# Optimization experiments

Measured on AMD Instinct MI355X. Metric: run time of the kernel, lower is better.

Reference implementation:

```python
import jax, jax.numpy as jnp
import numpy as np

B, C, H, W = 2, 512, 32, 32
HEADS = 8      # attention heads
GROUPS = 8     # offset groups (defaults to heads)
DH = 64        # dim_head
DF = 4         # downsample_factor
OFF_SCALE = 4.0
EPS = 1e-5


def _bn(t, gamma, beta):
    # eval-mode BatchNorm2d with running_mean=0, running_var=1
    s = gamma / jnp.sqrt(1.0 + EPS)
    return t * s[None, :, None, None] + beta[None, :, None, None]


def _gconv1x1(t, w):
    # grouped 1x1 conv (bias-free); w: (GROUPS, out_per_group, in_per_group)
    b, c, h, ww = t.shape
    o = jnp.einsum('bgci,goc->bgoi', t.reshape(b, GROUPS, c // GROUPS, h * ww), w)
    return o.reshape(b, GROUPS * w.shape[1], h, ww)


def _grid_sample(img, grid):
    # F.grid_sample: bilinear, padding_mode='zeros', align_corners=False
    # img: (N,Ci,Hi,Wi); grid: (N,Hg,Wg,2), grid[...,0]=x, grid[...,1]=y in [-1,1]
    N, Ci, Hi, Wi = img.shape
    gx = (grid[..., 0] + 1.0) * (Wi / 2.0) - 0.5
    gy = (grid[..., 1] + 1.0) * (Hi / 2.0) - 0.5
    x0 = jnp.floor(gx)
    y0 = jnp.floor(gy)
    wx = gx - x0
    wy = gy - y0

    def gather(im, ix, iy):
        valid = (ix >= 0) & (ix < Wi) & (iy >= 0) & (iy < Hi)
        ixc = jnp.clip(ix, 0, Wi - 1).astype(jnp.int32)
        iyc = jnp.clip(iy, 0, Hi - 1).astype(jnp.int32)
        return im[:, iyc, ixc] * valid[None].astype(im.dtype)

    def sample_one(im, x0, y0, wx, wy):
        v00 = gather(im, x0, y0)
        v01 = gather(im, x0 + 1, y0)
        v10 = gather(im, x0, y0 + 1)
        v11 = gather(im, x0 + 1, y0 + 1)
        wx = wx[None]
        wy = wy[None]
        return (v00 * (1 - wx) * (1 - wy) + v01 * wx * (1 - wy)
                + v10 * (1 - wx) * wy + v11 * wx * wy)

    return jax.vmap(sample_one)(img, x0, y0, wx, wy)


def _forward(x, bn1_g, bn1_b, bn2_g, bn2_b, qw, kw, vw, out_w, out_b,
             off_dw_w, off_dw_b, off_pw_w,
             cpb_w1, cpb_b1, cpb_w2, cpb_b2, cpb_w3, cpb_b3,
             mlp_w1, mlp_b1, mlp_w2, mlp_b2):
    b = x.shape[0]
    xn = _bn(x, bn1_g, bn1_b)
    # ---- deformable attention ----
    q = _gconv1x1(xn, qw)                                   # (b, 512, H, W)
    qg = q.reshape(b * GROUPS, DH, H, W)
    # to_offsets: depthwise conv k=6, s=4, p=1 -> GELU -> 1x1(64->2) -> tanh * offset_scale
    off = jax.lax.conv_general_dilated(
        qg, off_dw_w, (DF, DF), ((1, 1), (1, 1)),
        dimension_numbers=('NCHW', 'OIHW', 'NCHW'), feature_group_count=DH)
    off = jax.nn.gelu(off + off_dw_b[None, :, None, None], approximate=False)
    off = jnp.tanh(jnp.einsum('bchw,oc->bohw', off, off_pw_w)) * OFF_SCALE   # (b*G, 2, Hd, Wd)
    Hd, Wd = off.shape[-2], off.shape[-1]
    gy, gx = jnp.meshgrid(jnp.arange(Hd, dtype=x.dtype), jnp.arange(Wd, dtype=x.dtype), indexing='ij')
    vx = gx[None] + off[:, 0]
    vy = gy[None] + off[:, 1]
    # normalize_grid (lucidrains): first comp by (Hd-1), second by (Wd-1)
    nx = 2.0 * vx / max(Hd - 1, 1) - 1.0
    ny = 2.0 * vy / max(Wd - 1, 1) - 1.0
    vgrid_scaled = jnp.stack((nx, ny), axis=-1)             # (b*G, Hd, Wd, 2)
    kv = _grid_sample(xn.reshape(b * GROUPS, DH, H, W), vgrid_scaled)
    kv = kv.reshape(b, GROUPS * DH, Hd, Wd)
    k = _gconv1x1(kv, kw)
    v = _gconv1x1(kv, vw)
    scale = DH ** -0.5
    qh = q.reshape(b, HEADS, DH, H * W).transpose(0, 1, 3, 2) * scale    # (b,h,i,d)
    kh = k.reshape(b, HEADS, DH, Hd * Wd).transpose(0, 1, 3, 2)          # (b,h,j,d)
    vh = v.reshape(b, HEADS, DH, Hd * Wd).transpose(0, 1, 3, 2)
    # continuous relative position bias (CPB)
    qgy, qgx = jnp.meshgrid(jnp.arange(H, dtype=x.dtype), jnp.arange(W, dtype=x.dtype), indexing='ij')
    grid_q = jnp.stack((2.0 * qgx / max(H - 1, 1) - 1.0,
                        2.0 * qgy / max(W - 1, 1) - 1.0), axis=-1).reshape(1, H * W, 2)
    grid_kv = vgrid_scaled.reshape(b * GROUPS, Hd * Wd, 2)
    pos = grid_q[:, :, None, :] - grid_kv[:, None, :, :]    # (b*G, i, j, 2)
    bias = jnp.sign(pos) * jnp.log1p(jnp.abs(pos))
    bias = jax.nn.relu(bias @ cpb_w1 + cpb_b1)
    bias = jax.nn.relu(bias @ cpb_w2 + cpb_b2)
    bias = (bias @ cpb_w3 + cpb_b3).reshape(b, GROUPS, H * W, Hd * Wd)   # heads//groups == 1
    sim = jnp.einsum('bhid,bhjd->bhij', qh, kh) + bias
    attn = jax.nn.softmax(sim, axis=-1)
    out = jnp.einsum('bhij,bhjd->bhid', attn, vh)
    out = out.transpose(0, 1, 3, 2).reshape(b, HEADS * DH, H, W)
    out = jnp.einsum('bchw,oc->bohw', out, out_w) + out_b[None, :, None, None]
    x = x + out
    # ---- conv1x1 MLP ----
    xn2 = _bn(x, bn2_g, bn2_b)
    h1 = jax.nn.gelu(jnp.einsum('bchw,oc->bohw', xn2, mlp_w1) + mlp_b1[None, :, None, None],
                     approximate=False)
    return x + jnp.einsum('bchw,oc->bohw', h1, mlp_w2) + mlp_b2[None, :, None, None]


def setup_inputs():
    ks = jax.random.split(jax.random.key(0), 16)
    w = lambda k, shape: jax.random.normal(k, shape, dtype=jnp.float32) * 0.02
    return {
        'x': jax.random.normal(ks[0], (B, C, H, W), dtype=jnp.float32),
        'bn1_g': jnp.ones((C,), jnp.float32),
        'bn1_b': jnp.zeros((C,), jnp.float32),
        'bn2_g': jnp.ones((C,), jnp.float32),
        'bn2_b': jnp.zeros((C,), jnp.float32),
        'qw': w(ks[1], (GROUPS, DH, C // GROUPS)),
        'kw': w(ks[2], (GROUPS, DH, C // GROUPS)),
        'vw': w(ks[3], (GROUPS, DH, C // GROUPS)),
        'out_w': w(ks[4], (C, HEADS * DH)),
        'out_b': jnp.zeros((C,), jnp.float32),
        'off_dw_w': w(ks[5], (DH, 1, 6, 6)),
        'off_dw_b': jnp.zeros((DH,), jnp.float32),
        'off_pw_w': w(ks[6], (2, DH)),
        'cpb_w1': w(ks[7], (2, 128)),
        'cpb_b1': jnp.zeros((128,), jnp.float32),
        'cpb_w2': w(ks[8], (128, 128)),
        'cpb_b2': jnp.zeros((128,), jnp.float32),
        'cpb_w3': w(ks[9], (128, 1)),
        'cpb_b3': jnp.zeros((1,), jnp.float32),
        'mlp_w1': w(ks[10], (4 * C, C)),
        'mlp_b1': jnp.zeros((4 * C,), jnp.float32),
        'mlp_w2': w(ks[11], (C, 4 * C)),
        'mlp_b2': jnp.zeros((C,), jnp.float32),
    }


def reference(x, bn1_g, bn1_b, bn2_g, bn2_b, qw, kw, vw, out_w, out_b,
              off_dw_w, off_dw_b, off_pw_w,
              cpb_w1, cpb_b1, cpb_w2, cpb_b2, cpb_w3, cpb_b3,
              mlp_w1, mlp_b1, mlp_w2, mlp_b2):
    return _forward(x, bn1_g, bn1_b, bn2_g, bn2_b, qw, kw, vw, out_w, out_b,
                    off_dw_w, off_dw_b, off_pw_w,
                    cpb_w1, cpb_b1, cpb_w2, cpb_b2, cpb_w3, cpb_b3,
                    mlp_w1, mlp_b1, mlp_w2, mlp_b2)
```

## Files before the change

kernel.cpp:

```cpp
#include <hip/hip_runtime.h>
#include <hip/hip_bf16.h>
#include <math.h>

#define BB 2
#define CC 512
#define HH 32
#define WW 32
#define HWP 1024
#define GG 8
#define DH 64
#define HD 8
#define WD 8
#define JJ 64
#define BG 16
#define EPS 1e-5f

typedef __attribute__((ext_vector_type(8))) short short8;
typedef __attribute__((ext_vector_type(4))) short s16x4;
typedef __attribute__((ext_vector_type(4))) float f32x4;
typedef __attribute__((ext_vector_type(4))) unsigned short u16x4;
typedef __attribute__((ext_vector_type(4))) unsigned int u32x4;

static __device__ __forceinline__ short f2bf(float x) {
    unsigned u = __builtin_bit_cast(unsigned, x);
    u += 0x7FFFu + ((u >> 16) & 1u);
    return (short)(u >> 16);
}
static __device__ __forceinline__ float bf2f(unsigned short h) {
    return __builtin_bit_cast(float, (unsigned)h << 16);
}

__global__ void k_wpack(const float* __restrict__ qw, const float* __restrict__ ow,
                        const float* __restrict__ w1, const float* __restrict__ w2,
                        const float* __restrict__ cw2, unsigned short* __restrict__ wp,
                        unsigned short* __restrict__ w2p) {
    int idx = blockIdx.x * 256 + threadIdx.x;
    if (idx < 2392064) {
        float v;
        if (idx < 32768) v = qw[idx];
        else if (idx < 294912) v = ow[idx - 32768];
        else if (idx < 1343488) v = w1[idx - 294912];
        else v = w2[idx - 1343488];
        wp[idx] = (unsigned short)f2bf(v);
    } else if (idx < 2408448) {
        int i2 = idx - 2392064;
        int k = i2 >> 7, n = i2 & 127;
        int dest = ((((n >> 4) * 4 + (k >> 5)) * 64) + (((k >> 3) & 3) * 16) + (n & 15)) * 8 + (k & 7);
        w2p[dest] = (unsigned short)f2bf(cw2[i2]);
    }
}

__global__ __launch_bounds__(256) void k_qgemm(
    const float* __restrict__ x, const float* __restrict__ g1,
    const float* __restrict__ b1, const unsigned short* __restrict__ qwp,
    unsigned short* __restrict__ qt) {
    __shared__ __align__(16) short As[64][72];
    __shared__ __align__(16) short Bs[64][72];
    int blk = blockIdx.x;
    int bg = blk >> 4, nt = blk & 15;
    int b = bg >> 3, g = bg & 7;
    int i0 = nt * 64;
    int tid = threadIdx.x, lane = tid & 63, wv = tid >> 6;
    int wm = (wv >> 1) * 32, wn = (wv & 1) * 32;
    int l15 = lane & 15, quad = lane >> 4;
    const float invs = 1.0f / sqrtf(1.0f + EPS);
    {
        int c4 = (tid & 15) * 4;
        int ob = tid >> 4;
#pragma unroll
        for (int p = 0; p < 4; p++) {
            int o = ob + p * 16;
            u16x4 v = *(const u16x4*)(qwp + (size_t)(g * 64 + o) * 64 + c4);
            *(u16x4*)&As[o][c4] = v;
        }
    }
    {
        int i4 = (tid & 15) * 4;
        int cb = tid >> 4;
#pragma unroll
        for (int p = 0; p < 4; p++) {
            int c = cb + p * 16;
            f32x4 v = *(const f32x4*)(x + (size_t)(b * CC + g * 64 + c) * HWP + i0 + i4);
            float sc = g1[g * 64 + c] * invs;
            float sh = b1[g * 64 + c];
            Bs[i4 + 0][c] = f2bf(fmaf(v.x, sc, sh));
            Bs[i4 + 1][c] = f2bf(fmaf(v.y, sc, sh));
            Bs[i4 + 2][c] = f2bf(fmaf(v.z, sc, sh));
            Bs[i4 + 3][c] = f2bf(fmaf(v.w, sc, sh));
        }
    }
    __syncthreads();
    f32x4 acc[2][2];
#pragma unroll
    for (int a = 0; a < 2; a++)
#pragma unroll
        for (int c = 0; c < 2; c++) acc[a][c] = (f32x4){0.f, 0.f, 0.f, 0.f};
#pragma unroll
    for (int ks = 0; ks < 2; ks++) {
        short8 af0 = *(const short8*)&As[wm + l15][ks * 32 + quad * 8];
        short8 af1 = *(const short8*)&As[wm + 16 + l15][ks * 32 + quad * 8];
        short8 bf0 = *(const short8*)&Bs[wn + l15][ks * 32 + quad * 8];
        short8 bf1 = *(const short8*)&Bs[wn + 16 + l15][ks * 32 + quad * 8];
        acc[0][0] = __builtin_amdgcn_mfma_f32_16x16x32_bf16(af0, bf0, acc[0][0], 0, 0, 0);
        acc[0][1] = __builtin_amdgcn_mfma_f32_16x16x32_bf16(af0, bf1, acc[0][1], 0, 0, 0);
        acc[1][0] = __builtin_amdgcn_mfma_f32_16x16x32_bf16(af1, bf0, acc[1][0], 0, 0, 0);
        acc[1][1] = __builtin_amdgcn_mfma_f32_16x16x32_bf16(af1, bf1, acc[1][1], 0, 0, 0);
    }
    __syncthreads();
#pragma unroll
    for (int im = 0; im < 2; im++)
#pragma unroll
        for (int r = 0; r < 4; r++) {
            int m = wm + im * 16 + quad * 4 + r;
#pragma unroll
            for (int in_ = 0; in_ < 2; in_++) {
                int n = wn + in_ * 16 + l15;
                As[n][m] = f2bf(acc[im][in_][r]);
            }
        }
    __syncthreads();
    {
        int n = tid >> 2;
        int c0 = (tid & 3) * 16;
        short8 a = *(const short8*)&As[n][c0];
        short8 c = *(const short8*)&As[n][c0 + 8];
        unsigned short* dst = qt + ((size_t)bg * 1024 + i0 + n) * 64 + c0;
        *(short8*)dst = a;
        *(short8*)(dst + 8) = c;
    }
}

__global__ __launch_bounds__(64) void k_offskv(
    const unsigned short* __restrict__ qt, const float* __restrict__ dww,
    const float* __restrict__ dwb, const float* __restrict__ pw,
    const float* __restrict__ x, const float* __restrict__ g1,
    const float* __restrict__ b1, const float* __restrict__ kw,
    const float* __restrict__ vw, float* __restrict__ vgrid,
    float* __restrict__ kk, float* __restrict__ vv) {
    __shared__ float sm[64];
    int blk = blockIdx.x;
    int bg = blk >> 6;
    int hd = (blk >> 3) & 7;
    int wd = blk & 7;
    int g = bg & 7, b = bg >> 3;
    int ch = threadIdx.x;
    const unsigned short* qb = qt + (size_t)bg * 65536;
    float acc = 0.f;
#pragma unroll
    for (int kh = 0; kh < 6; kh++) {
        int hin = hd * 4 - 1 + kh;
        if (hin < 0 || hin >= HH) continue;
#pragma unroll
        for (int kw_ = 0; kw_ < 6; kw_++) {
            int win = wd * 4 - 1 + kw_;
            if (win < 0 || win >= WW) continue;
            acc = fmaf(bf2f(qb[(hin * WW + win) * 64 + ch]), dww[ch * 36 + kh * 6 + kw_], acc);
        }
    }
    acc += dwb[ch];
    float ge = 0.5f * acc * (1.0f + erff(acc * 0.7071067811865475f));
    float p0 = ge * pw[ch];
    float p1 = ge * pw[64 + ch];
#pragma unroll
    for (int off = 32; off; off >>= 1) {
        p0 += __shfl_xor(p0, off);
        p1 += __shfl_xor(p1, off);
    }
    float nx = 2.0f * ((float)wd + tanhf(p0) * 4.0f) / 7.0f - 1.0f;
    float ny = 2.0f * ((float)hd + tanhf(p1) * 4.0f) / 7.0f - 1.0f;
    if (ch == 0) {
        vgrid[blk * 2] = nx;
        vgrid[blk * 2 + 1] = ny;
    }
    {
        int cg = g * 64 + ch;
        const float invs = 1.0f / sqrtf(1.0f + EPS);
        float s = g1[cg] * invs;
        float bv = b1[cg];
        float gx = (nx + 1.0f) * 16.0f - 0.5f;
        float gy = (ny + 1.0f) * 16.0f - 0.5f;
        float x0f = floorf(gx), y0f = floorf(gy);
        float wx = gx - x0f, wy = gy - y0f;
        int x0 = (int)x0f, y0 = (int)y0f;
        const float* im = x + (size_t)(b * CC + cg) * HWP;
        float sx = 0.f, sw = 0.f;
        float w00 = (1 - wx) * (1 - wy), w01 = wx * (1 - wy);
        float w10 = (1 - wx) * wy, w11 = wx * wy;
        if (x0 >= 0 && x0 < WW && y0 >= 0 && y0 < HH)                 { sx += w00 * im[y0 * WW + x0];           sw += w00; }
        if (x0 + 1 >= 0 && x0 + 1 < WW && y0 >= 0 && y0 < HH)         { sx += w01 * im[y0 * WW + x0 + 1];       sw += w01; }
        if (x0 >= 0 && x0 < WW && y0 + 1 >= 0 && y0 + 1 < HH)         { sx += w10 * im[(y0 + 1) * WW + x0];     sw += w10; }
        if (x0 + 1 >= 0 && x0 + 1 < WW && y0 + 1 >= 0 && y0 + 1 < HH) { sx += w11 * im[(y0 + 1) * WW + x0 + 1]; sw += w11; }
        sm[ch] = s * sx + bv * sw;
    }
    __syncthreads();
    int j = blk & 63;
    const float* kwr = kw + (size_t)(g * 64 + ch) * 64;
    const float* vwr = vw + (size_t)(g * 64 + ch) * 64;
    float ak = 0.f, av = 0.f;
#pragma unroll
    for (int c = 0; c < 64; c++) {
        float tv = sm[c];
        ak = fmaf(tv, kwr[c], ak);
        av = fmaf(tv, vwr[c], av);
    }
    kk[(size_t)bg * 4096 + j * 64 + ch] = ak;
    vv[(size_t)bg * 4096 + j * 64 + ch] = av;
}

__global__ __launch_bounds__(256) void k_cpb(
    const float* __restrict__ vgrid, const unsigned short* __restrict__ w2p,
    const float* __restrict__ w1, const float* __restrict__ b1,
    const float* __restrict__ b2, const float* __restrict__ w3,
    const float* __restrict__ b3, unsigned short* __restrict__ bias) {
    __shared__ __align__(16) short w2fs[16384];
    int tid = threadIdx.x;
    {
        const u32x4* src = (const u32x4*)w2p;
        u32x4* dst = (u32x4*)w2fs;
        for (int c = tid; c < 2048; c += 256) dst[c] = src[c];
    }
    float bias3 = b3[0];
    __syncthreads();

    int lane = tid & 63;
    int wv = tid >> 6;
    int l15 = lane & 15;
    int quad = lane >> 4;

#pragma unroll 1
    for (int it = 0; it < 4; it++) {
        int p = (blockIdx.x * 4 + it) * 4 + wv;
        int pu = __builtin_amdgcn_readfirstlane(p);
        int cofs = (int)((unsigned)pu >> 20);
        int bg = p >> 11;
        int i = (p >> 1) & 1023;
        int jbase = (p & 1) * 32;
        int hi = i >> 5, wi = i & 31;
        float qx = 2.0f * (float)wi / 31.0f - 1.0f;
        float qy = 2.0f * (float)hi / 31.0f - 1.0f;

        int jA = jbase + l15;
        float gkxA = vgrid[(bg * 64 + jA) * 2];
        float gkyA = vgrid[(bg * 64 + jA) * 2 + 1];
        float gkxB = vgrid[(bg * 64 + jA + 16) * 2];
        float gkyB = vgrid[(bg * 64 + jA + 16) * 2 + 1];
        float p0 = qx - gkxA, p1 = qy - gkyA;
        float s0a = copysignf(log1pf(fabsf(p0)), p0);
        float s1a = copysignf(log1pf(fabsf(p1)), p1);
        p0 = qx - gkxB; p1 = qy - gkyB;
        float s0b = copysignf(log1pf(fabsf(p0)), p0);
        float s1b = copysignf(log1pf(fabsf(p1)), p1);

        short8 hA[4], hB[4];
#pragma unroll
        for (int kc = 0; kc < 4; kc++) {
            f32x4 cu0 = *(const f32x4*)(w1 + cofs + kc * 32 + quad * 8);
            f32x4 cu1 = *(const f32x4*)(w1 + cofs + kc * 32 + quad * 8 + 4);
            f32x4 cv0 = *(const f32x4*)(w1 + cofs + 128 + kc * 32 + quad * 8);
            f32x4 cv1 = *(const f32x4*)(w1 + cofs + 128 + kc * 32 + quad * 8 + 4);
            f32x4 cb0 = *(const f32x4*)(b1 + cofs + kc * 32 + quad * 8);
            f32x4 cb1 = *(const f32x4*)(b1 + cofs + kc * 32 + quad * 8 + 4);
            u32x4 pa, pb;
#pragma unroll
            for (int j2 = 0; j2 < 4; j2++) {
                int e0 = 2 * j2, e1 = 2 * j2 + 1;
                float u0 = (e0 < 4) ? cu0[e0] : cu1[e0 - 4];
                float u1 = (e1 < 4) ? cu0[e1] : cu1[e1 - 4];
                float v0 = (e0 < 4) ? cv0[e0] : cv1[e0 - 4];
                float v1 = (e1 < 4) ? cv0[e1] : cv1[e1 - 4];
                float c0 = (e0 < 4) ? cb0[e0] : cb1[e0 - 4];
                float c1 = (e1 < 4) ? cb0[e1] : cb1[e1 - 4];
                unsigned a0 = __builtin_bit_cast(unsigned,
                    fmaxf(fmaf(s0a, u0, fmaf(s1a, v0, c0)), 0.f)) + 0x8000u;
                unsigned a1 = __builtin_bit_cast(unsigned,
                    fmaxf(fmaf(s0a, u1, fmaf(s1a, v1, c1)), 0.f)) + 0x8000u;
                pa[j2] = __builtin_amdgcn_perm(a1, a0, 0x07060302);
                unsigned b0 = __builtin_bit_cast(unsigned,
                    fmaxf(fmaf(s0b, u0, fmaf(s1b, v0, c0)), 0.f)) + 0x8000u;
                unsigned b1_ = __builtin_bit_cast(unsigned,
                    fmaxf(fmaf(s0b, u1, fmaf(s1b, v1, c1)), 0.f)) + 0x8000u;
                pb[j2] = __builtin_amdgcn_perm(b1_, b0, 0x07060302);
            }
            hA[kc] = __builtin_bit_cast(short8, pa);
            hB[kc] = __builtin_bit_cast(short8, pb);
        }

        float psumA = 0.f, psumB = 0.f;
#pragma unroll 2
        for (int nt = 0; nt < 8; nt++) {
            f32x4 accA = (f32x4){0.f, 0.f, 0.f, 0.f};
            f32x4 accB = (f32x4){0.f, 0.f, 0.f, 0.f};
#pragma unroll
            for (int kc = 0; kc < 4; kc++) {
                short8 af = *(const short8*)(w2fs + (((nt * 4 + kc) * 64) + lane) * 8);
                accA = __builtin_amdgcn_mfma_f32_16x16x32_bf16(af, hA[kc], accA, 0, 0, 0);
                accB = __builtin_amdgcn_mfma_f32_16x16x32_bf16(af, hB[kc], accB, 0, 0, 0);
            }
            f32x4 b2q = *(const f32x4*)(b2 + cofs + nt * 16 + quad * 4);
            f32x4 w3q = *(const f32x4*)(w3 + cofs + nt * 16 + quad * 4);
#pragma unroll
            for (int r = 0; r < 4; r++) {
                psumA = fmaf(fmaxf(accA[r] + b2q[r], 0.f), w3q[r], psumA);
                psumB = fmaf(fmaxf(accB[r] + b2q[r], 0.f), w3q[r], psumB);
            }
        }
        psumA += __shfl_xor(psumA, 16);
        psumA += __shfl_xor(psumA, 32);
        psumB += __shfl_xor(psumB, 16);
        psumB += __shfl_xor(psumB, 32);
        if (quad == 0) {
            bias[(size_t)(p * 2 + 0) * 16 + l15] = (unsigned short)f2bf(psumA + bias3);
            bias[(size_t)(p * 2 + 1) * 16 + l15] = (unsigned short)f2bf(psumB + bias3);
        }
    }
}

__global__ __launch_bounds__(256) void k_attn(
    const unsigned short* __restrict__ qt, const float* __restrict__ kk,
    const float* __restrict__ vv, const unsigned short* __restrict__ bias,
    unsigned short* __restrict__ ao) {
    __shared__ __align__(16) short Ks[64][72];
    __shared__ __align__(16) short Vt[64][72];
    __shared__ __align__(16) short Qs[64][72];
    __shared__ __align__(16) short Ps[4][16][72];
    int blk = blockIdx.x;
    int bg = blk >> 4;
    int chunk = blk & 15;
    int i0 = chunk * 64;
    int b = bg >> 3, g = bg & 7;
    int tid = threadIdx.x, lane = tid & 63, wv = tid >> 6;
    int l15 = lane & 15, quad = lane >> 4;

    const float* kbase = kk + (size_t)bg * 4096;
    const float* vbase = vv + (size_t)bg * 4096;
#pragma unroll
    for (int it = 0; it < 4; it++) {
        int e4 = it * 1024 + tid * 4;
        int j = e4 >> 6, d = e4 & 63;
        f32x4 k4 = *(const f32x4*)(kbase + e4);
        s16x4 s = {f2bf(k4.x), f2bf(k4.y), f2bf(k4.z), f2bf(k4.w)};
        *(s16x4*)&Ks[j][d] = s;
        f32x4 v4 = *(const f32x4*)(vbase + e4);
        Vt[d + 0][j] = f2bf(v4.x);
        Vt[d + 1][j] = f2bf(v4.y);
        Vt[d + 2][j] = f2bf(v4.z);
        Vt[d + 3][j] = f2bf(v4.w);
    }
    {
        const unsigned short* qtb = qt + ((size_t)bg * 1024 + i0) * 64;
#pragma unroll
        for (int it = 0; it < 4; it++) {
            int e4 = it * 1024 + tid * 4;
            int i = e4 >> 6, d = e4 & 63;
            u16x4 v = *(const u16x4*)(qtb + e4);
            *(u16x4*)&Qs[i][d] = v;
        }
    }
    __syncthreads();

    int iw = wv * 16;
    f32x4 Sacc[4];
#pragma unroll
    for (int nt = 0; nt < 4; nt++) Sacc[nt] = (f32x4){0.f, 0.f, 0.f, 0.f};
#pragma unroll
    for (int ks = 0; ks < 2; ks++) {
        short8 aq = *(const short8*)&Qs[iw + l15][quad * 8 + ks * 32];
#pragma unroll
        for (int nt = 0; nt < 4; nt++) {
            short8 bk = *(const short8*)&Ks[nt * 16 + l15][quad * 8 + ks * 32];
            Sacc[nt] = __builtin_amdgcn_mfma_f32_16x16x32_bf16(aq, bk, Sacc[nt], 0, 0, 0);
        }
    }
    const unsigned short* bp = bias + ((size_t)bg * 1024 + i0 + iw + quad * 4) * 64 + l15;
    float Sv[4][4];
#pragma unroll
    for (int nt = 0; nt < 4; nt++)
#pragma unroll
        for (int r = 0; r < 4; r++)
            Sv[nt][r] = fmaf(Sacc[nt][r], 0.125f, bf2f(bp[r * 64 + nt * 16]));
#pragma unroll
    for (int r = 0; r < 4; r++) {
        float m = fmaxf(fmaxf(Sv[0][r], Sv[1][r]), fmaxf(Sv[2][r], Sv[3][r]));
        m = fmaxf(m, __shfl_xor(m, 1));
        m = fmaxf(m, __shfl_xor(m, 2));
        m = fmaxf(m, __shfl_xor(m, 4));
        m = fmaxf(m, __shfl_xor(m, 8));
        float l = 0.f;
#pragma unroll
        for (int nt = 0; nt < 4; nt++) { Sv[nt][r] = expf(Sv[nt][r] - m); l += Sv[nt][r]; }
        l += __shfl_xor(l, 1);
        l += __shfl_xor(l, 2);
        l += __shfl_xor(l, 4);
        l += __shfl_xor(l, 8);
        float inv = 1.0f / l;
#pragma unroll
        for (int nt = 0; nt < 4; nt++)
            Ps[wv][quad * 4 + r][nt * 16 + l15] = f2bf(Sv[nt][r] * inv);
    }
    f32x4 Oacc[4];
#pragma unroll
    for (int nt = 0; nt < 4; nt++) Oacc[nt] = (f32x4){0.f, 0.f, 0.f, 0.f};
#pragma unroll
    for (int ks = 0; ks < 2; ks++) {
        short8 ap = *(const short8*)&Ps[wv][l15][quad * 8 + ks * 32];
#pragma unroll
        for (int nt = 0; nt < 4; nt++) {
            short8 bv = *(const short8*)&Vt[nt * 16 + l15][quad * 8 + ks * 32];
            Oacc[nt] = __builtin_amdgcn_mfma_f32_16x16x32_bf16(ap, bv, Oacc[nt], 0, 0, 0);
        }
    }
    __syncthreads();
#pragma unroll
    for (int nt = 0; nt < 4; nt++) {
        s16x4 o4 = {f2bf(Oacc[nt][0]), f2bf(Oacc[nt][1]), f2bf(Oacc[nt][2]), f2bf(Oacc[nt][3])};
        *(s16x4*)&Qs[nt * 16 + l15][iw + quad * 4] = o4;
    }
    __syncthreads();
    {
        int d = tid >> 2;
        int ic = (tid & 3) * 16;
        short8 a = *(const short8*)&Qs[d][ic];
        short8 c = *(const short8*)&Qs[d][ic + 8];
        unsigned short* dst = ao + (size_t)(b * CC + g * 64 + d) * HWP + i0 + ic;
        *(short8*)dst = a;
        *(short8*)(dst + 8) = c;
    }
}

template<int EPI, int KD, int BK, int MT>
__global__ __launch_bounds__(256) void k_gemm(
    const unsigned short* __restrict__ A, const unsigned short* __restrict__ Bh,
    const float* __restrict__ resid, const float* __restrict__ bias,
    void* __restrict__ outp, unsigned short* __restrict__ out2,
    const float* __restrict__ bns, const float* __restrict__ bnb) {
    constexpr int MM = MT * 64;
    constexpr int KV4 = BK / 4;
    constexpr int RP = 256 / KV4;
    constexpr int NA = 64 / RP;
    constexpr int NB = BK / 16;
    __shared__ __align__(16) short As[64][BK + 8];
    __shared__ __align__(16) short Bs[64][BK + 8];
    int tid = threadIdx.x;
    int blk = blockIdx.x;
    int mt = blk & (MT - 1);
    int nb = blk / MT;
    int bb = nb >> 4, nt = nb & 15;
    int m0 = mt * 64, i0 = nt * 64;
    int lane = tid & 63, wv = tid >> 6;
    int wm = (wv >> 1) * 32, wn = (wv & 1) * 32;
    int l15 = lane & 15, quad = lane >> 4;
    const unsigned short* Af = A + (size_t)m0 * KD;
    const float invs = 1.0f / sqrtf(1.0f + EPS);
    int kk4 = (tid & (KV4 - 1)) * 4;
    int myb = tid / KV4;
    int i4 = (tid & 15) * 4;
    int kyb8 = (tid >> 4) * NB;

    f32x4 acc[2][2];
#pragma unroll
    for (int a = 0; a < 2; a++)
#pragma unroll
        for (int c = 0; c < 2; c++) acc[a][c] = (f32x4){0.f, 0.f, 0.f, 0.f};

    u16x4 ra[NA], rb[NB];
#pragma unroll
    for (int p = 0; p < NA; p++)
        ra[p] = *(const u16x4*)(Af + (size_t)(myb + p * RP) * KD + kk4);
#pragma unroll
    for (int p = 0; p < NB; p++)
        rb[p] = *(const u16x4*)(Bh + (size_t)bb * KD * HWP + (size_t)(kyb8 + p) * HWP + i0 + i4);

    for (int k0 = 0; k0 < KD; k0 += BK) {
        __syncthreads();
#pragma unroll
        for (int p = 0; p < NA; p++)
            *(u16x4*)&As[myb + p * RP][kk4] = ra[p];
#pragma unroll
        for (int q = 0; q < 4; q++) {
            u32x4 w;
#pragma unroll
            for (int j = 0; j < 4; j++) {
                unsigned lo = ((const unsigned*)&rb[2 * j])[q >> 1];
                unsigned hi = ((const unsigned*)&rb[2 * j + 1])[q >> 1];
                w[j] = (q & 1) ? __builtin_amdgcn_perm(hi, lo, 0x07060302)
                               : __builtin_amdgcn_perm(hi, lo, 0x05040100);
            }
            *(u32x4*)&Bs[i4 + q][kyb8] = w;
        }
        __syncthreads();
        int kn = k0 + BK;
        if (kn < KD) {
#pragma unroll
            for (int p = 0; p < NA; p++)
                ra[p] = *(const u16x4*)(Af + (size_t)(myb + p * RP) * KD + kn + kk4);
#pragma unroll
            for (int p = 0; p < NB; p++)
                rb[p] = *(const u16x4*)(Bh + (size_t)bb * KD * HWP + (size_t)(kn + kyb8 + p) * HWP + i0 + i4);
        }
#pragma unroll
        for (int ks = 0; ks < BK / 32; ks++) {
            short8 af0 = *(const short8*)&As[wm + l15][ks * 32 + quad * 8];
            short8 af1 = *(const short8*)&As[wm + 16 + l15][ks * 32 + quad * 8];
            short8 bf0 = *(const short8*)&Bs[wn + l15][ks * 32 + quad * 8];
            short8 bf1 = *(const short8*)&Bs[wn + 16 + l15][ks * 32 + quad * 8];
            acc[0][0] = __builtin_amdgcn_mfma_f32_16x16x32_bf16(af0, bf0, acc[0][0], 0, 0, 0);
            acc[0][1] = __builtin_amdgcn_mfma_f32_16x16x32_bf16(af0, bf1, acc[0][1], 0, 0, 0);
            acc[1][0] = __builtin_amdgcn_mfma_f32_16x16x32_bf16(af1, bf0, acc[1][0], 0, 0, 0);
            acc[1][1] = __builtin_amdgcn_mfma_f32_16x16x32_bf16(af1, bf1, acc[1][1], 0, 0, 0);
        }
    }

    float* outF = (float*)outp;
    unsigned short* outH = (unsigned short*)outp;
#pragma unroll
    for (int im = 0; im < 2; im++) {
#pragma unroll
        for (int r = 0; r < 4; r++) {
            int m = m0 + wm + im * 16 + quad * 4 + r;
            float bv = bias[m];
#pragma unroll
            for (int in_ = 0; in_ < 2; in_++) {
                int n = i0 + wn + in_ * 16 + l15;
                size_t idx = ((size_t)bb * MM + m) * HWP + n;
                float v = acc[im][in_][r] + bv;
                if constexpr (EPI == 1) {
                    float ge = 0.5f * v * (1.0f + erff(v * 0.7071067811865475f));
                    outH[idx] = (unsigned short)f2bf(ge);
                } else if constexpr (EPI == 3) {
                    float vr = v + resid[idx];
                    outF[idx] = vr;
                    out2[idx] = (unsigned short)f2bf(fmaf(vr, bns[m] * invs, bnb[m]));
                } else {
                    outF[idx] = v + resid[idx];
                }
            }
        }
    }
}

extern "C" void kernel_launch(void* const* d_in, const int* in_sizes, int n_in,
                              void* d_out, int out_size, void* d_ws, size_t ws_size,
                              hipStream_t stream) {
    const float* x      = (const float*)d_in[0];
    const float* bn1_g  = (const float*)d_in[1];
    const float* bn1_b  = (const float*)d_in[2];
    const float* bn2_g  = (const float*)d_in[3];
    const float* bn2_b  = (const float*)d_in[4];
    const float* qw     = (const float*)d_in[5];
    const float* kw     = (const float*)d_in[6];
    const float* vw     = (const float*)d_in[7];
    const float* out_w  = (const float*)d_in[8];
    const float* out_b  = (const float*)d_in[9];
    const float* off_dw_w = (const float*)d_in[10];
    const float* off_dw_b = (const float*)d_in[11];
    const float* off_pw_w = (const float*)d_in[12];
    const float* cpb_w1 = (const float*)d_in[13];
    const float* cpb_b1 = (const float*)d_in[14];
    const float* cpb_w2 = (const float*)d_in[15];
    const float* cpb_b2 = (const float*)d_in[16];
    const float* cpb_w3 = (const float*)d_in[17];
    const float* cpb_b3 = (const float*)d_in[18];
    const float* mlp_w1 = (const float*)d_in[19];
    const float* mlp_b1 = (const float*)d_in[20];
    const float* mlp_w2 = (const float*)d_in[21];
    const float* mlp_b2 = (const float*)d_in[22];

    float* ws = (float*)d_ws;
    unsigned short* qt = (unsigned short*)(ws + 1048576);
    float* vgrid = ws + 2097152;
    float* kk    = ws + 2164736;
    float* vv    = ws + 2230272;
    unsigned short* w2p = (unsigned short*)(ws + 2295808);
    unsigned short* ao  = (unsigned short*)(ws + 2312192);
    unsigned short* xn2 = (unsigned short*)(ws + 2836480);
    float* xo    = ws + 3360768;
    float* h1of  = ws + 4409344;
    unsigned short* biasb = (unsigned short*)h1of;
    unsigned short* h1o = (unsigned short*)h1of;
    unsigned short* wp  = (unsigned short*)(ws + 6506496);
    unsigned short* qwp  = wp;
    unsigned short* owp  = wp + 32768;
    unsigned short* w1p  = wp + 294912;
    unsigned short* w2mp = wp + 1343488;

    hipLaunchKernelGGL(k_wpack, dim3(9408), dim3(256), 0, stream,
                       qw, out_w, mlp_w1, mlp_w2, cpb_w2, wp, w2p);
    hipLaunchKernelGGL(k_qgemm, dim3(256), dim3(256), 0, stream, x, bn1_g, bn1_b, qwp, qt);
    hipLaunchKernelGGL(k_offskv, dim3(1024), dim3(64), 0, stream,
                       qt, off_dw_w, off_dw_b, off_pw_w, x, bn1_g, bn1_b, kw, vw,
                       vgrid, kk, vv);
    hipLaunchKernelGGL(k_cpb, dim3(2048), dim3(256), 0, stream,
                       vgrid, w2p, cpb_w1, cpb_b1, cpb_b2, cpb_w3, cpb_b3, biasb);
    hipLaunchKernelGGL(k_attn, dim3(256), dim3(256), 0, stream, qt, kk, vv, biasb, ao);
    k_gemm<3, 512, 128, 8><<<dim3(256), dim3(256), 0, stream>>>(
        owp, ao, x, out_b, xo, xn2, bn2_g, bn2_b);
    k_gemm<1, 512, 128, 32><<<dim3(1024), dim3(256), 0, stream>>>(
        w1p, xn2, nullptr, mlp_b1, h1o, nullptr, nullptr, nullptr);
    k_gemm<2, 2048, 128, 8><<<dim3(256), dim3(256), 0, stream>>>(
        w2mp, h1o, xo, mlp_b2, d_out, nullptr, nullptr, nullptr);
}
```

Before: 239.5 us.

## Transpose k/v/depthwise weights for coalesced reads and store K/V as bf16

Result: faster. 234.2 us (-2.2%).

```diff
diff --git a/kernel.cpp b/kernel.cpp
--- a/kernel.cpp
+++ b/kernel.cpp
@@ -32,8 +32,11 @@
 
 __global__ void k_wpack(const float* __restrict__ qw, const float* __restrict__ ow,
                         const float* __restrict__ w1, const float* __restrict__ w2,
-                        const float* __restrict__ cw2, unsigned short* __restrict__ wp,
-                        unsigned short* __restrict__ w2p) {
+                        const float* __restrict__ cw2, const float* __restrict__ kw,
+                        const float* __restrict__ vw, const float* __restrict__ dww,
+                        unsigned short* __restrict__ wp, unsigned short* __restrict__ w2p,
+                        float* __restrict__ kwt, float* __restrict__ vwt,
+                        float* __restrict__ dwt) {
     int idx = blockIdx.x * 256 + threadIdx.x;
     if (idx < 2392064) {
         float v;
@@ -47,6 +50,18 @@
         int k = i2 >> 7, n = i2 & 127;
         int dest = ((((n >> 4) * 4 + (k >> 5)) * 64) + (((k >> 3) & 3) * 16) + (n & 15)) * 8 + (k & 7);
         w2p[dest] = (unsigned short)f2bf(cw2[i2]);
+    } else if (idx < 2441216) {
+        int i2 = idx - 2408448;
+        int o = i2 & 63, c = (i2 >> 6) & 63, g = i2 >> 12;
+        kwt[i2] = kw[(size_t)(g * 64 + o) * 64 + c];
+    } else if (idx < 2473984) {
+        int i2 = idx - 2441216;
+        int o = i2 & 63, c = (i2 >> 6) & 63, g = i2 >> 12;
+        vwt[i2] = vw[(size_t)(g * 64 + o) * 64 + c];
+    } else if (idx < 2476288) {
+        int i2 = idx - 2473984;
+        int ch = i2 & 63, k = i2 >> 6;
+        dwt[i2] = dww[ch * 36 + k];
     }
 }
 
@@ -131,12 +146,12 @@
 }
 
 __global__ __launch_bounds__(64) void k_offskv(
-    const unsigned short* __restrict__ qt, const float* __restrict__ dww,
+    const unsigned short* __restrict__ qt, const float* __restrict__ dwt,
     const float* __restrict__ dwb, const float* __restrict__ pw,
     const float* __restrict__ x, const float* __restrict__ g1,
-    const float* __restrict__ b1, const float* __restrict__ kw,
-    const float* __restrict__ vw, float* __restrict__ vgrid,
-    float* __restrict__ kk, float* __restrict__ vv) {
+    const float* __restrict__ b1, const float* __restrict__ kwt,
+    const float* __restrict__ vwt, float* __restrict__ vgrid,
+    unsigned short* __restrict__ kkh, unsigned short* __restrict__ vvh) {
     __shared__ float sm[64];
     int blk = blockIdx.x;
     int bg = blk >> 6;
@@ -154,7 +169,8 @@
         for (int kw_ = 0; kw_ < 6; kw_++) {
             int win = wd * 4 - 1 + kw_;
             if (win < 0 || win >= WW) continue;
-            acc = fmaf(bf2f(qb[(hin * WW + win) * 64 + ch]), dww[ch * 36 + kh * 6 + kw_], acc);
+            acc = fmaf(bf2f(qb[(hin * WW + win) * 64 + ch]),
+                       dwt[(kh * 6 + kw_) * 64 + ch], acc);
         }
     }
     acc += dwb[ch];
@@ -194,17 +210,17 @@
     }
     __syncthreads();
     int j = blk & 63;
-    const float* kwr = kw + (size_t)(g * 64 + ch) * 64;
-    const float* vwr = vw + (size_t)(g * 64 + ch) * 64;
+    const float* kwr = kwt + g * 4096 + ch;
+    const float* vwr = vwt + g * 4096 + ch;
     float ak = 0.f, av = 0.f;
 #pragma unroll
     for (int c = 0; c < 64; c++) {
         float tv = sm[c];
-        ak = fmaf(tv, kwr[c], ak);
-        av = fmaf(tv, vwr[c], av);
-    }
-    kk[(size_t)bg * 4096 + j * 64 + ch] = ak;
-    vv[(size_t)bg * 4096 + j * 64 + ch] = av;
+        ak = fmaf(tv, kwr[c * 64], ak);
+        av = fmaf(tv, vwr[c * 64], av);
+    }
+    kkh[(size_t)bg * 4096 + j * 64 + ch] = (unsigned short)f2bf(ak);
+    vvh[(size_t)bg * 4096 + j * 64 + ch] = (unsigned short)f2bf(av);
 }
 
 __global__ __launch_bounds__(256) void k_cpb(
@@ -316,8 +332,8 @@
 }
 
 __global__ __launch_bounds__(256) void k_attn(
-    const unsigned short* __restrict__ qt, const float* __restrict__ kk,
-    const float* __restrict__ vv, const unsigned short* __restrict__ bias,
+    const unsigned short* __restrict__ qt, const unsigned short* __restrict__ kkh,
+    const unsigned short* __restrict__ vvh, const unsigned short* __restrict__ bias,
     unsigned short* __restrict__ ao) {
     __shared__ __align__(16) short Ks[64][72];
     __shared__ __align__(16) short Vt[64][72];
@@ -331,20 +347,34 @@
     int tid = threadIdx.x, lane = tid & 63, wv = tid >> 6;
     int l15 = lane & 15, quad = lane >> 4;
 
-    const float* kbase = kk + (size_t)bg * 4096;
-    const float* vbase = vv + (size_t)bg * 4096;
-#pragma unroll
-    for (int it = 0; it < 4; it++) {
-        int e4 = it * 1024 + tid * 4;
-        int j = e4 >> 6, d = e4 & 63;
-        f32x4 k4 = *(const f32x4*)(kbase + e4);
-        s16x4 s = {f2bf(k4.x), f2bf(k4.y), f2bf(k4.z), f2bf(k4.w)};
-        *(s16x4*)&Ks[j][d] = s;
-        f32x4 v4 = *(const f32x4*)(vbase + e4);
-        Vt[d + 0][j] = f2bf(v4.x);
-        Vt[d + 1][j] = f2bf(v4.y);
-        Vt[d + 2][j] = f2bf(v4.z);
-        Vt[d + 3][j] = f2bf(v4.w);
+    const unsigned short* kbase = kkh + (size_t)bg * 4096;
+    const unsigned short* vbase = vvh + (size_t)bg * 4096;
+#pragma unroll
+    for (int it = 0; it < 2; it++) {
+        int e8 = (it * 256 + tid) * 8;
+        int j = e8 >> 6, d = e8 & 63;
+        u32x4 v = *(const u32x4*)(kbase + e8);
+        *(u32x4*)&Ks[j][d] = v;
+    }
+    if (tid < 128) {
+        int d0 = (tid & 15) * 4;
+        int jb = (tid >> 4) * 8;
+        u16x4 rb[8];
+#pragma unroll
+        for (int p = 0; p < 8; p++)
+            rb[p] = *(const u16x4*)(vbase + (jb + p) * 64 + d0);
+#pragma unroll
+        for (int q = 0; q < 4; q++) {
+            u32x4 w;
+#pragma unroll
+            for (int jj = 0; jj < 4; jj++) {
+                unsigned lo = ((const unsigned*)&rb[2 * jj])[q >> 1];
+                unsigned hi = ((const unsigned*)&rb[2 * jj + 1])[q >> 1];
+                w[jj] = (q & 1) ? __builtin_amdgcn_perm(hi, lo, 0x07060302)
+                                : __builtin_amdgcn_perm(hi, lo, 0x05040100);
+            }
+            *(u32x4*)&Vt[d0 + q][jb] = w;
+        }
     }
     {
         const unsigned short* qtb = qt + ((size_t)bg * 1024 + i0) * 64;
@@ -568,8 +598,8 @@
     float* ws = (float*)d_ws;
     unsigned short* qt = (unsigned short*)(ws + 1048576);
     float* vgrid = ws + 2097152;
-    float* kk    = ws + 2164736;
-    float* vv    = ws + 2230272;
+    unsigned short* kkh = (unsigned short*)(ws + 2164736);
+    unsigned short* vvh = (unsigned short*)(ws + 2230272);
     unsigned short* w2p = (unsigned short*)(ws + 2295808);
     unsigned short* ao  = (unsigned short*)(ws + 2312192);
     unsigned short* xn2 = (unsigned short*)(ws + 2836480);
@@ -582,16 +612,20 @@
     unsigned short* owp  = wp + 32768;
     unsigned short* w1p  = wp + 294912;
     unsigned short* w2mp = wp + 1343488;
-
-    hipLaunchKernelGGL(k_wpack, dim3(9408), dim3(256), 0, stream,
-                       qw, out_w, mlp_w1, mlp_w2, cpb_w2, wp, w2p);
+    float* kwt = ws + 7702528;
+    float* vwt = ws + 7735296;
+    float* dwt = ws + 7768064;
+
+    hipLaunchKernelGGL(k_wpack, dim3(9673), dim3(256), 0, stream,
+                       qw, out_w, mlp_w1, mlp_w2, cpb_w2, kw, vw, off_dw_w,
+                       wp, w2p, kwt, vwt, dwt);
     hipLaunchKernelGGL(k_qgemm, dim3(256), dim3(256), 0, stream, x, bn1_g, bn1_b, qwp, qt);
     hipLaunchKernelGGL(k_offskv, dim3(1024), dim3(64), 0, stream,
-                       qt, off_dw_w, off_dw_b, off_pw_w, x, bn1_g, bn1_b, kw, vw,
-                       vgrid, kk, vv);
+                       qt, dwt, off_dw_b, off_pw_w, x, bn1_g, bn1_b, kwt, vwt,
+                       vgrid, kkh, vvh);
     hipLaunchKernelGGL(k_cpb, dim3(2048), dim3(256), 0, stream,
                        vgrid, w2p, cpb_w1, cpb_b1, cpb_b2, cpb_w3, cpb_b3, biasb);
-    hipLaunchKernelGGL(k_attn, dim3(256), dim3(256), 0, stream, qt, kk, vv, biasb, ao);
+    hipLaunchKernelGGL(k_attn, dim3(256), dim3(256), 0, stream, qt, kkh, vvh, biasb, ao);
     k_gemm<3, 512, 128, 8><<<dim3(256), dim3(256), 0, stream>>>(
         owp, ao, x, out_b, xo, xn2, bn2_g, bn2_b);
     k_gemm<1, 512, 128, 32><<<dim3(1024), dim3(256), 0, stream>>>(
```
